# Kernel tuning notes

Hardware: AMD Instinct MI355X
Metric: run time of the kernel (lower is better)

Reference implementation:

```python
import jax, jax.numpy as jnp
import numpy as np

NUM_HEADS = 8
ATTN_BALANCE = 0.5
EPS = 1e-4  # eps in normalize()


def mp_linear(x, w, gain):
    # MP_Conv with kernel=(1,1): per-output-channel RMS weight renorm then scale.
    # normalize(w): w / (eps + ||w_row|| / sqrt(fan_in)); then * gain / sqrt(fan_in)
    fan_in = w.shape[1]
    n = jnp.linalg.norm(w.astype(jnp.float32), axis=1, keepdims=True)  # (out,1)
    wn = w / (EPS + n / np.sqrt(fan_in))
    wn = wn * (gain / np.sqrt(fan_in))
    return x @ wn.T


def setup_inputs() -> dict:
    key = jax.random.key(0)
    ks = jax.random.split(key, 6)
    B, S, E = 8, 1024, 1024
    H = NUM_HEADS
    return {
        "query": jax.random.normal(ks[0], (B, S, E), jnp.float32),
        "gain_s": jnp.ones((), jnp.float32),
        "gain_t": jnp.ones((), jnp.float32),
        "q_w": jax.random.normal(ks[1], (E, E), jnp.float32),
        "k_w": jax.random.normal(ks[2], (E, E), jnp.float32),
        "v_w": jax.random.normal(ks[3], (E, E), jnp.float32),
        "o_w": jax.random.normal(ks[4], (E, E), jnp.float32),
        "rel_pos_bias": 0.01 * jax.random.normal(ks[5], (H, S, S), jnp.float32),
    }


def reference(query, gain_s, gain_t, q_w, k_w, v_w, o_w, rel_pos_bias):
    # time_dim=0 so the time-dependent branches are inactive; gain_t unused.
    B, S, E = query.shape
    H = NUM_HEADS
    hd = E // H
    # MP projections (1x1 conv == per-position linear), split heads -> (B,H,S,hd)
    q = mp_linear(query, q_w, gain_s).reshape(B, S, H, hd).transpose(0, 2, 1, 3)
    k = mp_linear(query, k_w, gain_s).reshape(B, S, H, hd).transpose(0, 2, 1, 3)
    v = mp_linear(query, v_w, gain_s).reshape(B, S, H, hd).transpose(0, 2, 1, 3)
    # (B,H,S,S) scores, scaled, plus learned relative position bias (seq_len == seq_ln)
    scores = jnp.einsum("bhsd,bhtd->bhst", q, k) / np.sqrt(hd) + rel_pos_bias[None]
    attn = jax.nn.softmax(scores, axis=-1)
    o = jnp.einsum("bhst,bhtd->bhsd", attn, v)
    o = o.transpose(0, 2, 1, 3).reshape(B, S, E)
    out = mp_linear(o, o_w, gain_s)
    # mp_sum residual: lerp(res, out, t) / sqrt((1-t)^2 + t^2)
    t = ATTN_BALANCE
    return (query * (1.0 - t) + out * t) / np.sqrt((1.0 - t) ** 2 + t ** 2)
```

## Files before the change

### kernel.cpp

```cpp
#include <hip/hip_runtime.h>
#include <hip/hip_bf16.h>
#include <math.h>


typedef __attribute__((ext_vector_type(4))) float f32x4;
typedef __attribute__((ext_vector_type(16))) float f32x16;
typedef __attribute__((ext_vector_type(4))) short s16x4;
typedef __attribute__((ext_vector_type(8))) short s16x8;

__device__ __forceinline__ short f2bf(float f) {
  union { __hip_bfloat16 h; short s; } u;
  u.h = __float2bfloat16(f);
  return u.s;
}
__device__ __forceinline__ float bf2f(short s) {
  union { short s; __hip_bfloat16 h; } u;
  u.s = s;
  return __bfloat162float(u.h);
}
__device__ __forceinline__ f32x4 mfma16(s16x8 a, s16x8 b, f32x4 c) {
  return __builtin_amdgcn_mfma_f32_16x16x32_bf16(a, b, c, 0, 0, 0);
}
__device__ __forceinline__ f32x16 mfma32(s16x8 a, s16x8 b, f32x16 c) {
  return __builtin_amdgcn_mfma_f32_32x32x16_bf16(a, b, c, 0, 0, 0);
}

typedef __attribute__((address_space(1))) const unsigned int* as1_u32p;
typedef __attribute__((address_space(3))) unsigned int* as3_u32p;
__device__ __forceinline__ void g2l16(const short* g, short* l) {
  __builtin_amdgcn_global_load_lds((as1_u32p)g, (as3_u32p)l, 16, 0, 0);
}

#define ASM_VMCNT0 asm volatile("s_waitcnt vmcnt(0)" ::: "memory")
#define ASM_LGKM0  asm volatile("s_waitcnt lgkmcnt(0)" ::: "memory")
#define SFENCE     __builtin_amdgcn_sched_barrier(0)
#define BARRIER    __builtin_amdgcn_s_barrier()

__global__ __launch_bounds__(256) void k_wnorm(const float* __restrict__ qw, const float* __restrict__ kw,
                                               const float* __restrict__ vw, const float* __restrict__ ow,
                                               const float* __restrict__ gain, short* __restrict__ wn) {
  const int r = blockIdx.x;
  const int mat = r >> 10;
  const float* W = mat == 0 ? qw : mat == 1 ? kw : mat == 2 ? vw : ow;
  const float* src = W + (size_t)(r & 1023) * 1024;
  const int tid = threadIdx.x;
  f32x4 v = *(const f32x4*)&src[tid * 4];
  float s = v[0]*v[0] + v[1]*v[1] + v[2]*v[2] + v[3]*v[3];
  __shared__ float red[256];
  red[tid] = s; __syncthreads();
  for (int off = 128; off > 0; off >>= 1) {
    if (tid < off) red[tid] += red[tid + off];
    __syncthreads();
  }
  const float scale = gain[0] / (0.0032f + sqrtf(red[0]));
  s16x4 o;
  o[0] = f2bf(v[0]*scale); o[1] = f2bf(v[1]*scale);
  o[2] = f2bf(v[2]*scale); o[3] = f2bf(v[3]*scale);
  *(s16x4*)&wn[(size_t)r * 1024 + tid * 4] = o;
}

__global__ __launch_bounds__(256) void k_cvt(const float* __restrict__ in, short* __restrict__ out, int n4) {
  int idx = blockIdx.x * 256 + threadIdx.x;
  int stride = gridDim.x * 256;
  for (int i = idx; i < n4; i += stride) {
    f32x4 v = ((const f32x4*)in)[i];
    s16x4 o;
    o[0] = f2bf(v[0]); o[1] = f2bf(v[1]); o[2] = f2bf(v[2]); o[3] = f2bf(v[3]);
    ((s16x4*)out)[i] = o;
  }
}

__global__ __launch_bounds__(256) void k_scaleb(const float* __restrict__ in, short* __restrict__ out, int n4) {
  const float L2E = 1.4426950408889634f;
  int idx = blockIdx.x * 256 + threadIdx.x;
  int stride = gridDim.x * 256;
  for (int i = idx; i < n4; i += stride) {
    f32x4 v = ((const f32x4*)in)[i];
    s16x4 o;
    o[0] = f2bf(v[0]*L2E); o[1] = f2bf(v[1]*L2E);
    o[2] = f2bf(v[2]*L2E); o[3] = f2bf(v[3]*L2E);
    ((s16x4*)out)[i] = o;
  }
}

#define GEMM_K_LOOP(XPTR, WPTR)                                                      \
  const int srw = lane >> 3;                                  \
  const int ssl = lane & 7;                                            \
  const int ql7 = ql & 7;                                                            \
  {                                                                                  \
    _Pragma("unroll")                                                                \
    for (int i = 0; i < 4; i++) {                                                    \
      const int row = i * 32 + w * 8 + srw;                                          \
      g2l16(&XPTR[(size_t)(m0 + row) * 1024 + ((ssl ^ srw) << 3)],                   \
            &Al[0][(i * 32 + w * 8) * 64]);                                          \
      g2l16(&WPTR[(size_t)(n0 + row) * 1024 + ((ssl ^ srw) << 3)],                   \
            &Bl[0][(i * 32 + w * 8) * 64]);                                          \
    }                                                                                \
    ASM_VMCNT0; SFENCE; BARRIER; SFENCE;                                             \
    int bi = 0;                                                                      \
    for (int t = 0; t < 16; ++t) {                                                   \
      if (t < 15) {                                                                  \
        const int k1 = (t + 1) * 64;                                                 \
        _Pragma("unroll")                                                            \
        for (int i = 0; i < 4; i++) {                                                \
          const int row = i * 32 + w * 8 + srw;                                      \
          g2l16(&XPTR[(size_t)(m0 + row) * 1024 + k1 + ((ssl ^ srw) << 3)],          \
                &Al[bi ^ 1][(i * 32 + w * 8) * 64]);                                 \
          g2l16(&WPTR[(size_t)(n0 + row) * 1024 + k1 + ((ssl ^ srw) << 3)],          \
                &Bl[bi ^ 1][(i * 32 + w * 8) * 64]);                                 \
        }                                                                            \
      }                                                                              \
      const char* alp = (const char*)&Al[bi][0];                                     \
      const char* blp = (const char*)&Bl[bi][0];                                     \
      __builtin_amdgcn_s_setprio(1);                                                 \
      _Pragma("unroll")                                                              \
      for (int kc = 0; kc < 2; ++kc) {                                               \
        s16x8 af[4], bfr[4];                                                         \
        _Pragma("unroll")                                                            \
        for (int i = 0; i < 4; i++) {                                                \
          const int rA = wm * 64 + i * 16 + ql;                                      \
          af[i] = *(const s16x8*)(alp + rA * 128 +                                   \
                                  ((kc * 64 + 16 * hi) ^ (ql7 << 4)));               \
        }                                                                            \
        _Pragma("unroll")                                                            \
        for (int j = 0; j < 4; j++) {                                                \
          const int rB = wn_ * 64 + j * 16 + ql;                                     \
          bfr[j] = *(const s16x8*)(blp + rB * 128 +                                  \
                                   ((kc * 64 + 16 * hi) ^ (ql7 << 4)));              \
        }                                                                            \
        _Pragma("unroll")                                                            \
        for (int i = 0; i < 4; i++)                                                  \
          _Pragma("unroll")                                                          \
          for (int j = 0; j < 4; j++) acc[i][j] = mfma16(af[i], bfr[j], acc[i][j]);  \
      }                                                                              \
      __builtin_amdgcn_s_setprio(0);                                                 \
      ASM_VMCNT0; SFENCE; BARRIER; SFENCE;                                           \
      bi ^= 1;                                                                       \
    }                                                                                \
  }

__global__ __launch_bounds__(256) void k_gemm_qkv(const short* __restrict__ X, const short* __restrict__ WN,
                                                  short* __restrict__ Qb, short* __restrict__ Kb,
                                                  short* __restrict__ Vt) {
  __shared__ short Al[2][128 * 64];
  __shared__ short Bl[2][128 * 64];
  const int z = blockIdx.z;
  const short* __restrict__ Wm = WN + (size_t)z * 1048576;
  const int m0 = blockIdx.x * 128, n0 = blockIdx.y * 128;
  const int tid = threadIdx.x, lane = tid & 63, w = tid >> 6;
  const int hi = lane >> 4, ql = lane & 15;
  const int wm = w >> 1, wn_ = w & 1;
  f32x4 acc[4][4];
#pragma unroll
  for (int i = 0; i < 4; i++)
#pragma unroll
    for (int j = 0; j < 4; j++) acc[i][j] = (f32x4){0.f, 0.f, 0.f, 0.f};
  GEMM_K_LOOP(X, Wm)
  short* Cl = &Al[0][0];
  if (z == 2) {
#pragma unroll
    for (int i = 0; i < 4; i++) {
#pragma unroll
      for (int j = 0; j < 4; j++) {
        int col = wn_ * 64 + j * 16 + ql;
        int rowb = wm * 64 + i * 16 + 4 * hi;
#pragma unroll
        for (int r = 0; r < 4; r++) Cl[col * 128 + rowb + r] = f2bf(acc[i][j][r]);
      }
    }
    __syncthreads();
    const int b = m0 >> 10, sb = (m0 & 1023);
#pragma unroll
    for (int it = 0; it < 8; ++it) {
      int idx = tid + it * 256;
      int dl = idx >> 4, c = idx & 15;
      int ng = n0 + dl, h = ng >> 7, d = ng & 127;
      *(s16x8*)&Vt[(size_t)((b * 8 + h) * 128 + d) * 1024 + sb + c * 8] =
          *(const s16x8*)&Cl[dl * 128 + c * 8];
    }
  } else {
    short* __restrict__ C = (z == 0) ? Qb : Kb;
#pragma unroll
    for (int i = 0; i < 4; i++) {
#pragma unroll
      for (int j = 0; j < 4; j++) {
        int col = wn_ * 64 + j * 16 + ql;
        int rowb = wm * 64 + i * 16 + 4 * hi;
#pragma unroll
        for (int r = 0; r < 4; r++) Cl[(rowb + r) * 128 + col] = f2bf(acc[i][j][r]);
      }
    }
    __syncthreads();
#pragma unroll
    for (int it = 0; it < 8; ++it) {
      int idx = tid + it * 256;
      int row = idx >> 4, c = idx & 15;
      *(s16x8*)&C[(size_t)(m0 + row) * 1024 + n0 + c * 8] = *(const s16x8*)&Cl[row * 128 + c * 8];
    }
  }
}

__global__ __launch_bounds__(256) void k_attn(const short* __restrict__ Qb, const short* __restrict__ Kb,
                                              const short* __restrict__ Vt, const short* __restrict__ B2,
                                              short* __restrict__ Ob) {
  __shared__ short lds[64 * 128 + 128 * 64];
  short* Kl = lds;
  short* Vl = lds + 64 * 128;
  int f = blockIdx.x + (blockIdx.y << 3);
  f = (f & 7) * 64 + (f >> 3);
  const int bh = f >> 3, b = bh >> 3, h = bh & 7;
  const int q0 = (f & 7) * 128;
  const int tid = threadIdx.x, w = tid >> 6, lane = tid & 63;
  const int l31 = lane & 31, hi2 = lane >> 5, sw = l31 & 7;
  const int qrow = q0 + w * 32 + l31;
  const short* __restrict__ qbase = Qb + (size_t)(b * 1024 + qrow) * 1024 + h * 128;
  s16x8 qf[8];
#pragma unroll
  for (int kc = 0; kc < 8; kc++) qf[kc] = *(const s16x8*)&qbase[kc * 16 + hi2 * 8];
  float lsum = 0.f;
  f32x16 acc[4];
#pragma unroll
  for (int db = 0; db < 4; db++)
#pragma unroll
    for (int r = 0; r < 16; r++) acc[db][r] = 0.f;
  const float sc2 = (float)(0.08838834764831845 * 1.4426950408889634);
  const int krow_ = tid >> 4, kslot = tid & 15;
  const int vrow_ = tid >> 3, vslot = tid & 7;
  const int vks = vslot >> 1, vm = vslot & 1;
  const short* __restrict__ Kg = Kb + (size_t)(b * 1024) * 1024 + h * 128;
  const short* __restrict__ Vg = Vt + (size_t)bh * 128 * 1024;
  const short* __restrict__ Bg = B2 + (size_t)(h * 1024 + qrow) * 1024;

  s16x8 krA[4], vrA[4], krB[4], vrB[4];
#define LOADT(KR, VR, T0)                                                              \
  do {                                                                                 \
    _Pragma("unroll")                                                                  \
    for (int i = 0; i < 4; i++)                                                        \
      KR[i] = *(const s16x8*)&Kg[(size_t)((T0) + i * 16 + krow_) * 1024 + kslot * 8];  \
    _Pragma("unroll")                                                                  \
    for (int i = 0; i < 4; i++)                                                        \
      VR[i] = *(const s16x8*)&Vg[(size_t)(i * 32 + vrow_) * 1024 + (T0) + vslot * 8];  \
  } while (0)

#define STAGE(KR, VR)                                                                  \
  do {                                                                                 \
    _Pragma("unroll")                                                                  \
    for (int i = 0; i < 4; i++) {                                                      \
      int row = i * 16 + krow_;                                                        \
      *(s16x8*)((char*)Kl + row * 256 + ((kslot ^ (row & 7)) << 4)) = KR[i];           \
    }                                                                                  \
    _Pragma("unroll")                                                                  \
    for (int i = 0; i < 4; i++) {                                                      \
      int row = i * 32 + vrow_;                                                        \
      char* vb = (char*)Vl + row * 128;                                                \
      s16x4 lo, hi4;                                                                   \
      lo[0] = VR[i][0]; lo[1] = VR[i][1]; lo[2] = VR[i][2]; lo[3] = VR[i][3];          \
      hi4[0] = VR[i][4]; hi4[1] = VR[i][5]; hi4[2] = VR[i][6]; hi4[3] = VR[i][7];      \
      *(s16x4*)(vb + (((vks * 2) ^ (row & 7)) << 4) + vm * 8) = lo;                    \
      *(s16x4*)(vb + (((vks * 2 + 1) ^ (row & 7)) << 4) + vm * 8) = hi4;               \
    }                                                                                  \
  } while (0)

#define COMPUTE(T0)                                                                    \
  do {                                                                                 \
    s16x4 br[8];                           \
    _Pragma("unroll")                                                                  \
    for (int tb = 0; tb < 2; tb++)                                                     \
      _Pragma("unroll")                                                                \
      for (int u = 0; u < 4; u++)                                                      \
        br[tb * 4 + u] = *(const s16x4*)&Bg[(T0) + tb * 32 + u * 8 + 4 * hi2];         \
    f32x16 st[2];                                                                      \
    __builtin_amdgcn_s_setprio(1);                                                     \
    _Pragma("unroll")                                                                  \
    for (int tb = 0; tb < 2; tb++) {                                                   \
      _Pragma("unroll")                                                                \
      for (int r = 0; r < 16; r++) st[tb][r] = 0.f;                                    \
      _Pragma("unroll")                                                                \
      for (int kc = 0; kc < 8; kc++) {                                                 \
        s16x8 kf = *(const s16x8*)((const char*)Kl + (tb * 32 + l31) * 256 +           \
                                   (((kc * 2 + hi2) ^ sw) << 4));                      \
        st[tb] = mfma32(kf, qf[kc], st[tb]);                                           \
      }                                                                                \
    }                                                                                  \
    __builtin_amdgcn_s_setprio(0);                                                     \
    _Pragma("unroll")                                                                  \
    for (int tb = 0; tb < 2; tb++)                                                     \
      _Pragma("unroll")                                                                \
      for (int r = 0; r < 16; r++) {                                                   \
        float e = exp2f(fmaf(st[tb][r], sc2, bf2f(br[tb * 4 + (r >> 2)][r & 3])));     \
        st[tb][r] = e;                                                                 \
        lsum += e;                                                                     \
      }                                                                                \
    s16x8 pf[4];                  \
    _Pragma("unroll")                                                                  \
    for (int ks = 0; ks < 4; ks++)                                                     \
      _Pragma("unroll")                                                                \
      for (int e = 0; e < 8; e++)                                                      \
        pf[ks][e] = f2bf(st[ks >> 1][(e & 3) + 8 * (ks & 1) + 4 * (e >> 2)]);          \
    __builtin_amdgcn_s_setprio(1);                                                     \
    _Pragma("unroll")                                                                  \
    for (int db = 0; db < 4; db++)                                                     \
      _Pragma("unroll")                                                                \
      for (int ks = 0; ks < 4; ks++) {                                                 \
        s16x8 vf = *(const s16x8*)((const char*)Vl + (db * 32 + l31) * 128 +           \
                                   (((ks * 2 + hi2) ^ sw) << 4));                      \
        acc[db] = mfma32(vf, pf[ks], acc[db]);                                         \
      }                                                                                \
    __builtin_amdgcn_s_setprio(0);                                                     \
  } while (0)

  LOADT(krA, vrA, 0);
  for (int ih = 0; ih < 8; ++ih) {
    const int t0 = ih * 128;
    ASM_VMCNT0; SFENCE;
    STAGE(krA, vrA);
    LOADT(krB, vrB, t0 + 64);
    ASM_LGKM0; SFENCE; BARRIER; SFENCE;
    COMPUTE(t0);
    BARRIER; SFENCE;
    ASM_VMCNT0; SFENCE;
    STAGE(krB, vrB);
    if (ih < 7) LOADT(krA, vrA, t0 + 128);
    ASM_LGKM0; SFENCE; BARRIER; SFENCE;
    COMPUTE(t0 + 64);
    BARRIER; SFENCE;
  }
  lsum += __shfl_xor(lsum, 32);
  const float invl = 1.f / lsum;
  __syncthreads();
  short* Ol = lds;
  const int qloc = w * 32 + l31, qs = qloc & 7;
#pragma unroll
  for (int db = 0; db < 4; db++) {
#pragma unroll
    for (int u = 0; u < 4; u++) {
      int d0 = db * 32 + u * 8 + 4 * hi2;
      s16x4 v;
      v[0] = f2bf(acc[db][4 * u + 0] * invl);
      v[1] = f2bf(acc[db][4 * u + 1] * invl);
      v[2] = f2bf(acc[db][4 * u + 2] * invl);
      v[3] = f2bf(acc[db][4 * u + 3] * invl);
      *(s16x4*)((char*)Ol + qloc * 256 + (((d0 >> 3) ^ qs) << 4) + (d0 & 7) * 2) = v;
    }
  }
  __syncthreads();
#pragma unroll
  for (int it = 0; it < 8; ++it) {
    int idx = tid + it * 256;
    int row = idx >> 4, c = idx & 15;
    s16x8 vv = *(const s16x8*)((const char*)Ol + row * 256 + ((c ^ (row & 7)) << 4));
    *(s16x8*)&Ob[(size_t)(b * 1024 + q0 + row) * 1024 + h * 128 + c * 8] = vv;
  }
#undef LOADT
#undef STAGE
#undef COMPUTE
}

__global__ __launch_bounds__(256) void k_gemm_o(const short* __restrict__ X, const short* __restrict__ Wm,
                                                const float* __restrict__ Qin, float* __restrict__ Out) {
  __shared__ short Al[2][128 * 64];
  __shared__ short Bl[2][128 * 64];
  const int m0 = blockIdx.x * 128, n0 = blockIdx.y * 128;
  const int tid = threadIdx.x, lane = tid & 63, w = tid >> 6;
  const int hi = lane >> 4, ql = lane & 15;
  const int wm = w >> 1, wn_ = w & 1;
  f32x4 acc[4][4];
#pragma unroll
  for (int i = 0; i < 4; i++)
#pragma unroll
    for (int j = 0; j < 4; j++) acc[i][j] = (f32x4){0.f, 0.f, 0.f, 0.f};
  GEMM_K_LOOP(X, Wm)
#pragma unroll
  for (int i = 0; i < 4; i++) {
    int mg = m0 + wm * 64 + i * 16 + 4 * hi;
#pragma unroll
    for (int j = 0; j < 4; j++) {
      int ng = n0 + wn_ * 64 + j * 16 + ql;
#pragma unroll
      for (int r = 0; r < 4; r++) {
        size_t idx = (size_t)(mg + r) * 1024 + ng;
        Out[idx] = (Qin[idx] + acc[i][j][r]) * 0.7071067811865476f;
      }
    }
  }
}

extern "C" void kernel_launch(void* const* d_in, const int* in_sizes, int n_in,
                              void* d_out, int out_size, void* d_ws, size_t ws_size,
                              hipStream_t stream) {
  (void)in_sizes; (void)n_in; (void)out_size; (void)ws_size;
  const float* query = (const float*)d_in[0];
  const float* gain_s = (const float*)d_in[1];
  const float* qw = (const float*)d_in[3];
  const float* kw = (const float*)d_in[4];
  const float* vw = (const float*)d_in[5];
  const float* ow = (const float*)d_in[6];
  const float* bias = (const float*)d_in[7];
  float* out = (float*)d_out;

  short* ws = (short*)d_ws;
  short* s_wn = ws;
  short* s_x  = s_wn + 4 * 1048576;
  short* s_B2 = s_x + 8388608;
  short* s_Q  = s_B2 + 8388608;
  short* s_K  = s_Q + 8388608;
  short* s_Vt = s_K + 8388608;
  short* s_O  = s_x;

  k_wnorm<<<dim3(4096), dim3(256), 0, stream>>>(qw, kw, vw, ow, gain_s, s_wn);
  k_cvt<<<dim3(2048), dim3(256), 0, stream>>>(query, s_x, 2097152);
  k_scaleb<<<dim3(2048), dim3(256), 0, stream>>>(bias, s_B2, 2097152);
  k_gemm_qkv<<<dim3(64, 8, 3), dim3(256), 0, stream>>>(s_x, s_wn, s_Q, s_K, s_Vt);
  k_attn<<<dim3(8, 64), dim3(256), 0, stream>>>(s_Q, s_K, s_Vt, s_B2, s_O);
  k_gemm_o<<<dim3(64, 8), dim3(256), 0, stream>>>(s_O, s_wn + 3 * 1048576, query, out);
}
```

Baseline: 311.4 us.

## Fuse prep kernels into one launch and deepen GEMM prefetch to two tiles

Merges the weight-normalisation, query conversion and bias-scaling kernels into one launch that dispatches on block index, removing two kernel launches and the gaps between them. The GEMM K-loop is rewritten so the tile two steps ahead is prefetched into the buffer just consumed. It waits with vmcnt(8) instead of draining all loads, which gives more load/compute overlap. The cost is an extra barrier per iteration, because a buffer is refilled only after every wave has finished computing on it.

```diff
diff --git a/kernel.cpp b/kernel.cpp
--- a/kernel.cpp
+++ b/kernel.cpp
@@ -32,112 +32,105 @@
 }
 
 #define ASM_VMCNT0 asm volatile("s_waitcnt vmcnt(0)" ::: "memory")
+#define ASM_VMCNT8 asm volatile("s_waitcnt vmcnt(8)" ::: "memory")
 #define ASM_LGKM0  asm volatile("s_waitcnt lgkmcnt(0)" ::: "memory")
 #define SFENCE     __builtin_amdgcn_sched_barrier(0)
 #define BARRIER    __builtin_amdgcn_s_barrier()
 
-__global__ __launch_bounds__(256) void k_wnorm(const float* __restrict__ qw, const float* __restrict__ kw,
-                                               const float* __restrict__ vw, const float* __restrict__ ow,
-                                               const float* __restrict__ gain, short* __restrict__ wn) {
-  const int r = blockIdx.x;
-  const int mat = r >> 10;
-  const float* W = mat == 0 ? qw : mat == 1 ? kw : mat == 2 ? vw : ow;
-  const float* src = W + (size_t)(r & 1023) * 1024;
-  const int tid = threadIdx.x;
-  f32x4 v = *(const f32x4*)&src[tid * 4];
-  float s = v[0]*v[0] + v[1]*v[1] + v[2]*v[2] + v[3]*v[3];
+__global__ __launch_bounds__(256) void k_prep(const float* __restrict__ qw, const float* __restrict__ kw,
+                                              const float* __restrict__ vw, const float* __restrict__ ow,
+                                              const float* __restrict__ gain, const float* __restrict__ query,
+                                              const float* __restrict__ bias, short* __restrict__ wn,
+                                              short* __restrict__ xq, short* __restrict__ b2) {
   __shared__ float red[256];
-  red[tid] = s; __syncthreads();
-  for (int off = 128; off > 0; off >>= 1) {
-    if (tid < off) red[tid] += red[tid + off];
-    __syncthreads();
-  }
-  const float scale = gain[0] / (0.0032f + sqrtf(red[0]));
-  s16x4 o;
-  o[0] = f2bf(v[0]*scale); o[1] = f2bf(v[1]*scale);
-  o[2] = f2bf(v[2]*scale); o[3] = f2bf(v[3]*scale);
-  *(s16x4*)&wn[(size_t)r * 1024 + tid * 4] = o;
-}
-
-__global__ __launch_bounds__(256) void k_cvt(const float* __restrict__ in, short* __restrict__ out, int n4) {
-  int idx = blockIdx.x * 256 + threadIdx.x;
-  int stride = gridDim.x * 256;
-  for (int i = idx; i < n4; i += stride) {
-    f32x4 v = ((const f32x4*)in)[i];
+  const int bid = blockIdx.x, tid = threadIdx.x;
+  if (bid < 4096) {
+    const int mat = bid >> 10;
+    const float* W = mat == 0 ? qw : mat == 1 ? kw : mat == 2 ? vw : ow;
+    const float* src = W + (size_t)(bid & 1023) * 1024;
+    f32x4 v = *(const f32x4*)&src[tid * 4];
+    float s = v[0]*v[0] + v[1]*v[1] + v[2]*v[2] + v[3]*v[3];
+    red[tid] = s; __syncthreads();
+    for (int off = 128; off > 0; off >>= 1) {
+      if (tid < off) red[tid] += red[tid + off];
+      __syncthreads();
+    }
+    const float scale = gain[0] / (0.0032f + sqrtf(red[0]));
     s16x4 o;
-    o[0] = f2bf(v[0]); o[1] = f2bf(v[1]); o[2] = f2bf(v[2]); o[3] = f2bf(v[3]);
-    ((s16x4*)out)[i] = o;
-  }
-}
-
-__global__ __launch_bounds__(256) void k_scaleb(const float* __restrict__ in, short* __restrict__ out, int n4) {
-  const float L2E = 1.4426950408889634f;
-  int idx = blockIdx.x * 256 + threadIdx.x;
-  int stride = gridDim.x * 256;
-  for (int i = idx; i < n4; i += stride) {
-    f32x4 v = ((const f32x4*)in)[i];
-    s16x4 o;
-    o[0] = f2bf(v[0]*L2E); o[1] = f2bf(v[1]*L2E);
-    o[2] = f2bf(v[2]*L2E); o[3] = f2bf(v[3]*L2E);
-    ((s16x4*)out)[i] = o;
-  }
-}
-
-#define GEMM_K_LOOP(XPTR, WPTR)                                                      \
-  const int srw = lane >> 3;                                  \
-  const int ssl = lane & 7;                                            \
-  const int ql7 = ql & 7;                                                            \
-  {                                                                                  \
-    _Pragma("unroll")                                                                \
-    for (int i = 0; i < 4; i++) {                                                    \
-      const int row = i * 32 + w * 8 + srw;                                          \
-      g2l16(&XPTR[(size_t)(m0 + row) * 1024 + ((ssl ^ srw) << 3)],                   \
-            &Al[0][(i * 32 + w * 8) * 64]);                                          \
-      g2l16(&WPTR[(size_t)(n0 + row) * 1024 + ((ssl ^ srw) << 3)],                   \
-            &Bl[0][(i * 32 + w * 8) * 64]);                                          \
-    }                                                                                \
-    ASM_VMCNT0; SFENCE; BARRIER; SFENCE;                                             \
-    int bi = 0;                                                                      \
-    for (int t = 0; t < 16; ++t) {                                                   \
-      if (t < 15) {                                                                  \
-        const int k1 = (t + 1) * 64;                                                 \
-        _Pragma("unroll")                                                            \
-        for (int i = 0; i < 4; i++) {                                                \
-          const int row = i * 32 + w * 8 + srw;                                      \
-          g2l16(&XPTR[(size_t)(m0 + row) * 1024 + k1 + ((ssl ^ srw) << 3)],          \
-                &Al[bi ^ 1][(i * 32 + w * 8) * 64]);                                 \
-          g2l16(&WPTR[(size_t)(n0 + row) * 1024 + k1 + ((ssl ^ srw) << 3)],          \
-                &Bl[bi ^ 1][(i * 32 + w * 8) * 64]);                                 \
-        }                                                                            \
-      }                                                                              \
-      const char* alp = (const char*)&Al[bi][0];                                     \
-      const char* blp = (const char*)&Bl[bi][0];                                     \
-      __builtin_amdgcn_s_setprio(1);                                                 \
-      _Pragma("unroll")                                                              \
-      for (int kc = 0; kc < 2; ++kc) {                                               \
-        s16x8 af[4], bfr[4];                                                         \
-        _Pragma("unroll")                                                            \
-        for (int i = 0; i < 4; i++) {                                                \
-          const int rA = wm * 64 + i * 16 + ql;                                      \
-          af[i] = *(const s16x8*)(alp + rA * 128 +                                   \
-                                  ((kc * 64 + 16 * hi) ^ (ql7 << 4)));               \
-        }                                                                            \
-        _Pragma("unroll")                                                            \
-        for (int j = 0; j < 4; j++) {                                                \
-          const int rB = wn_ * 64 + j * 16 + ql;                                     \
-          bfr[j] = *(const s16x8*)(blp + rB * 128 +                                  \
-                                   ((kc * 64 + 16 * hi) ^ (ql7 << 4)));              \
-        }                                                                            \
-        _Pragma("unroll")                                                            \
-        for (int i = 0; i < 4; i++)                                                  \
-          _Pragma("unroll")                                                          \
-          for (int j = 0; j < 4; j++) acc[i][j] = mfma16(af[i], bfr[j], acc[i][j]);  \
-      }                                                                              \
-      __builtin_amdgcn_s_setprio(0);                                                 \
-      ASM_VMCNT0; SFENCE; BARRIER; SFENCE;                                           \
-      bi ^= 1;                                                                       \
-    }                                                                                \
-  }
+    o[0] = f2bf(v[0]*scale); o[1] = f2bf(v[1]*scale);
+    o[2] = f2bf(v[2]*scale); o[3] = f2bf(v[3]*scale);
+    *(s16x4*)&wn[(size_t)bid * 1024 + tid * 4] = o;
+  } else if (bid < 6144) {
+    for (int i = (bid - 4096) * 256 + tid; i < 2097152; i += 524288) {
+      f32x4 v = ((const f32x4*)query)[i];
+      s16x4 o;
+      o[0] = f2bf(v[0]); o[1] = f2bf(v[1]); o[2] = f2bf(v[2]); o[3] = f2bf(v[3]);
+      ((s16x4*)xq)[i] = o;
+    }
+  } else {
+    const float L2E = 1.4426950408889634f;
+    for (int i = (bid - 6144) * 256 + tid; i < 2097152; i += 524288) {
+      f32x4 v = ((const f32x4*)bias)[i];
+      s16x4 o;
+      o[0] = f2bf(v[0]*L2E); o[1] = f2bf(v[1]*L2E);
+      o[2] = f2bf(v[2]*L2E); o[3] = f2bf(v[3]*L2E);
+      ((s16x4*)b2)[i] = o;
+    }
+  }
+}
+
+__device__ __forceinline__ void gemm_core(const short* __restrict__ X, const short* __restrict__ W_,
+                                          int m0, int n0, int lane, int w, int hi, int ql,
+                                          int wm, int wn_, short Al[2][8192], short Bl[2][8192],
+                                          f32x4 acc[4][4]) {
+  const int srw = lane >> 3, ssl = lane & 7, ql7 = ql & 7;
+  auto stage8 = [&](int BI, int K0) {
+#pragma unroll
+    for (int i = 0; i < 4; i++) {
+      const int row = i * 32 + w * 8 + srw;
+      g2l16(&X[(size_t)(m0 + row) * 1024 + K0 + ((ssl ^ srw) << 3)],
+            &Al[BI][(i * 32 + w * 8) * 64]);
+      g2l16(&W_[(size_t)(n0 + row) * 1024 + K0 + ((ssl ^ srw) << 3)],
+            &Bl[BI][(i * 32 + w * 8) * 64]);
+    }
+  };
+  auto compute_tile = [&](int BI) {
+    const char* alp = (const char*)&Al[BI][0];
+    const char* blp = (const char*)&Bl[BI][0];
+    __builtin_amdgcn_s_setprio(1);
+#pragma unroll
+    for (int kc = 0; kc < 2; ++kc) {
+      s16x8 af[4], bfr[4];
+#pragma unroll
+      for (int i = 0; i < 4; i++) {
+        const int rA = wm * 64 + i * 16 + ql;
+        af[i] = *(const s16x8*)(alp + rA * 128 + ((kc * 64 + 16 * hi) ^ (ql7 << 4)));
+      }
+#pragma unroll
+      for (int j = 0; j < 4; j++) {
+        const int rB = wn_ * 64 + j * 16 + ql;
+        bfr[j] = *(const s16x8*)(blp + rB * 128 + ((kc * 64 + 16 * hi) ^ (ql7 << 4)));
+      }
+#pragma unroll
+      for (int i = 0; i < 4; i++)
+#pragma unroll
+        for (int j = 0; j < 4; j++) acc[i][j] = mfma16(af[i], bfr[j], acc[i][j]);
+    }
+    __builtin_amdgcn_s_setprio(0);
+  };
+  stage8(0, 0);
+  stage8(1, 64);
+  int bi = 0;
+  for (int t = 0; t < 15; ++t) {
+    ASM_VMCNT8; SFENCE; BARRIER; SFENCE;
+    compute_tile(bi);
+    SFENCE; BARRIER; SFENCE;
+    if (t < 14) stage8(bi, (t + 2) * 64);
+    bi ^= 1;
+  }
+  ASM_VMCNT0; SFENCE; BARRIER; SFENCE;
+  compute_tile(bi);
+}
 
 __global__ __launch_bounds__(256) void k_gemm_qkv(const short* __restrict__ X, const short* __restrict__ WN,
                                                   short* __restrict__ Qb, short* __restrict__ Kb,
@@ -155,7 +148,7 @@
   for (int i = 0; i < 4; i++)
 #pragma unroll
     for (int j = 0; j < 4; j++) acc[i][j] = (f32x4){0.f, 0.f, 0.f, 0.f};
-  GEMM_K_LOOP(X, Wm)
+  gemm_core(X, Wm, m0, n0, lane, w, hi, ql, wm, wn_, Al, Bl, acc);
   short* Cl = &Al[0][0];
   if (z == 2) {
 #pragma unroll
@@ -369,7 +362,7 @@
   for (int i = 0; i < 4; i++)
 #pragma unroll
     for (int j = 0; j < 4; j++) acc[i][j] = (f32x4){0.f, 0.f, 0.f, 0.f};
-  GEMM_K_LOOP(X, Wm)
+  gemm_core(X, Wm, m0, n0, lane, w, hi, ql, wm, wn_, Al, Bl, acc);
 #pragma unroll
   for (int i = 0; i < 4; i++) {
     int mg = m0 + wm * 64 + i * 16 + 4 * hi;
@@ -407,9 +400,7 @@
   short* s_Vt = s_K + 8388608;
   short* s_O  = s_x;
 
-  k_wnorm<<<dim3(4096), dim3(256), 0, stream>>>(qw, kw, vw, ow, gain_s, s_wn);
-  k_cvt<<<dim3(2048), dim3(256), 0, stream>>>(query, s_x, 2097152);
-  k_scaleb<<<dim3(2048), dim3(256), 0, stream>>>(bias, s_B2, 2097152);
+  k_prep<<<dim3(8192), dim3(256), 0, stream>>>(qw, kw, vw, ow, gain_s, query, bias, s_wn, s_x, s_B2);
   k_gemm_qkv<<<dim3(64, 8, 3), dim3(256), 0, stream>>>(s_x, s_wn, s_Q, s_K, s_Vt);
   k_attn<<<dim3(8, 64), dim3(256), 0, stream>>>(s_Q, s_K, s_Vt, s_B2, s_O);
   k_gemm_o<<<dim3(64, 8), dim3(256), 0, stream>>>(s_O, s_wn + 3 * 1048576, query, out);
```

Measured after the change: 296.5 us. 4.8% less time.
